# Performance work log

Hardware: AMD Instinct MI355X
Metric: run time of the kernel (lower is better)

## Reference

```python
import jax, jax.numpy as jnp
import numpy as np

B, S, EMBED, FFN, NQ = 8, 2048, 1024, 4096, 8

def setup_inputs() -> dict:
    key = jax.random.key(0)
    ks = jax.random.split(key, 6)
    return {
        "x": jax.random.normal(ks[0], (B, S, EMBED), dtype=jnp.float32),
        "theta": jax.random.normal(ks[1], (NQ,), dtype=jnp.float32),
        "W1": jax.random.normal(ks[2], (FFN, NQ), dtype=jnp.float32) * (1.0 / np.sqrt(NQ)),
        "b1": jax.random.normal(ks[3], (FFN,), dtype=jnp.float32) * 0.02,
        "W2": jax.random.normal(ks[4], (EMBED, FFN), dtype=jnp.float32) * (1.0 / np.sqrt(FFN)),
        "b2": jax.random.normal(ks[5], (EMBED,), dtype=jnp.float32) * 0.02,
    }

def reference(x, theta, W1, b1, W2, b2):
    # Quantum layer (product circuit, closed form): per qubit i,
    # |0> -RX(x_i)-> -RY(theta_i)->, <PauliZ> = cos(x_i) * cos(theta_i).
    nq = theta.shape[0]
    q = jnp.cos(x[..., :nq]) * jnp.cos(theta)        # [B,S,NQ]
    # dropout is identity in eval mode
    h = jax.nn.relu(jnp.einsum('bsq,fq->bsf', q, W1) + b1)  # [B,S,FFN]
    return jnp.einsum('bsf,ef->bse', h, W2) + b2            # [B,S,EMBED]
```

## Files before the change

### kernel.cpp

```cpp
#include <hip/hip_runtime.h>
#include <cstdint>
#include <cstddef>

#define AS1 __attribute__((address_space(1)))
#define AS3 __attribute__((address_space(3)))

typedef __bf16 bf16x8 __attribute__((ext_vector_type(8)));
typedef float  f32x16 __attribute__((ext_vector_type(16)));

#define MDIM 16384
#define NDIM 1024
#define KDIM 4096
#define NQ   8

#define BM 256
#define BN 256
#define BK 64

__global__ __launch_bounds__(256) void conv_w2_kernel(const float* __restrict__ W2,
                                                      __bf16* __restrict__ W2b) {
    size_t base = ((size_t)blockIdx.x * 256 + threadIdx.x) * 8;
    float4 a = *(const float4*)(W2 + base);
    float4 b = *(const float4*)(W2 + base + 4);
    bf16x8 v;
    v[0] = (__bf16)a.x; v[1] = (__bf16)a.y; v[2] = (__bf16)a.z; v[3] = (__bf16)a.w;
    v[4] = (__bf16)b.x; v[5] = (__bf16)b.y; v[6] = (__bf16)b.z; v[7] = (__bf16)b.w;
    *(bf16x8*)(W2b + base) = v;
}

#define QROWS 64
__global__ __launch_bounds__(256) void qh_kernel(const float* __restrict__ x,
                                                 const float* __restrict__ theta,
                                                 const float* __restrict__ W1,
                                                 const float* __restrict__ b1,
                                                 __bf16* __restrict__ H) {
    const int t  = threadIdx.x;
    const int f0 = blockIdx.y * 2048 + t * 8;
    const int r0 = blockIdx.x * QROWS;

    float w[8][8];
#pragma unroll
    for (int fr = 0; fr < 8; ++fr) {
        float4 a = *(const float4*)(W1 + (size_t)(f0 + fr) * NQ);
        float4 b = *(const float4*)(W1 + (size_t)(f0 + fr) * NQ + 4);
        w[fr][0] = a.x; w[fr][1] = a.y; w[fr][2] = a.z; w[fr][3] = a.w;
        w[fr][4] = b.x; w[fr][5] = b.y; w[fr][6] = b.z; w[fr][7] = b.w;
    }
    float bias[8];
    {
        float4 a = *(const float4*)(b1 + f0);
        float4 b = *(const float4*)(b1 + f0 + 4);
        bias[0] = a.x; bias[1] = a.y; bias[2] = a.z; bias[3] = a.w;
        bias[4] = b.x; bias[5] = b.y; bias[6] = b.z; bias[7] = b.w;
    }
    float ct[NQ];
#pragma unroll
    for (int i = 0; i < NQ; ++i) ct[i] = __cosf(theta[i]);

#pragma unroll 1
    for (int r = 0; r < QROWS; ++r) {
        const float* xr = x + (size_t)(r0 + r) * 1024;
        const float4 xa = *(const float4*)xr;
        const float4 xb = *(const float4*)(xr + 4);
        float q[8];
        q[0] = __cosf(xa.x) * ct[0]; q[1] = __cosf(xa.y) * ct[1];
        q[2] = __cosf(xa.z) * ct[2]; q[3] = __cosf(xa.w) * ct[3];
        q[4] = __cosf(xb.x) * ct[4]; q[5] = __cosf(xb.y) * ct[5];
        q[6] = __cosf(xb.z) * ct[6]; q[7] = __cosf(xb.w) * ct[7];
        bf16x8 o;
#pragma unroll
        for (int fr = 0; fr < 8; ++fr) {
            float a = bias[fr];
#pragma unroll
            for (int i = 0; i < 8; ++i) a += q[i] * w[fr][i];
            a = fmaxf(a, 0.f);
            o[fr] = (__bf16)a;
        }
        *(bf16x8*)(H + (size_t)(r0 + r) * KDIM + f0) = o;
    }
}

__global__ __launch_bounds__(256, 1) void gemm_bt_kernel(const __bf16* __restrict__ A,
                                                         const __bf16* __restrict__ B,
                                                         const float* __restrict__ bias,
                                                         float* __restrict__ C) {
    __shared__ __align__(16) __bf16 Al[BM * BK];
    __shared__ __align__(16) __bf16 Bl[BN * BK];

    const int tid  = threadIdx.x;
    const int wave = tid >> 6;
    const int lane = tid & 63;
    const int bm = blockIdx.x;
    const int bn = blockIdx.y;

    const int lr = lane >> 3;
    const int ul = (lane & 7) ^ lr;
    const __bf16* gA0 = A + (size_t)(bm * BM + wave * 64 + lr) * KDIM + ul * 8;
    const __bf16* gB0 = B + (size_t)(bn * BN + wave * 64 + lr) * KDIM + ul * 8;
    __bf16* lA0 = &Al[(wave * 64) * BK];
    __bf16* lB0 = &Bl[(wave * 64) * BK];

    const int fl = lane & 31;
    const int fq = lane >> 5;
    const int sw = fl & 7;
    const int wm = (wave & 1) * 128;
    const int wn = (wave >> 1) * 128;

    f32x16 acc[4][4] = {};

    for (int kt = 0; kt < KDIM; kt += BK) {
        __syncthreads();
#pragma unroll
        for (int c = 0; c < 8; ++c) {
            __builtin_amdgcn_global_load_lds((AS1 void*)(gA0 + (size_t)c * 8 * KDIM + kt),
                                             (AS3 void*)(lA0 + c * 8 * BK), 16, 0, 0);
            __builtin_amdgcn_global_load_lds((AS1 void*)(gB0 + (size_t)c * 8 * KDIM + kt),
                                             (AS3 void*)(lB0 + c * 8 * BK), 16, 0, 0);
        }
        __syncthreads();
#pragma unroll
        for (int t4 = 0; t4 < 4; ++t4) {
            const int u = ((t4 * 2 + fq) ^ sw) * 8;
            bf16x8 af[4], bfr[4];
#pragma unroll
            for (int i = 0; i < 4; ++i) {
                af[i]  = *(const bf16x8*)&Al[(wm + i * 32 + fl) * BK + u];
                bfr[i] = *(const bf16x8*)&Bl[(wn + i * 32 + fl) * BK + u];
            }
#pragma unroll
            for (int i = 0; i < 4; ++i)
#pragma unroll
                for (int j = 0; j < 4; ++j)
                    acc[i][j] = __builtin_amdgcn_mfma_f32_32x32x16_bf16(af[i], bfr[j], acc[i][j], 0, 0, 0);
        }
    }

    const int cm0 = bm * BM + wm;
    const int cn0 = bn * BN + wn;
#pragma unroll
    for (int j = 0; j < 4; ++j) {
        const int col = cn0 + j * 32 + fl;
        const float bv = bias[col];
#pragma unroll
        for (int i = 0; i < 4; ++i)
#pragma unroll
            for (int r = 0; r < 16; ++r) {
                const int row = cm0 + i * 32 + (r & 3) + 8 * (r >> 2) + 4 * fq;
                C[(size_t)row * NDIM + col] = acc[i][j][r] + bv;
            }
    }
}

extern "C" void kernel_launch(void* const* d_in, const int* in_sizes, int n_in,
                              void* d_out, int out_size, void* d_ws, size_t ws_size,
                              hipStream_t stream) {
    const float* x     = (const float*)d_in[0];
    const float* theta = (const float*)d_in[1];
    const float* W1    = (const float*)d_in[2];
    const float* b1    = (const float*)d_in[3];
    const float* W2    = (const float*)d_in[4];
    const float* b2    = (const float*)d_in[5];
    float* out = (float*)d_out;

    __bf16* H   = (__bf16*)d_ws;
    __bf16* W2b = (__bf16*)((char*)d_ws + (size_t)MDIM * KDIM * 2);

    conv_w2_kernel<<<(KDIM * NDIM) / (256 * 8), 256, 0, stream>>>(W2, W2b);
    qh_kernel<<<dim3(MDIM / QROWS, KDIM / 2048), 256, 0, stream>>>(x, theta, W1, b1, H);
    gemm_bt_kernel<<<dim3(MDIM / BM, NDIM / BN), 256, 0, stream>>>(H, W2b, b2, out);
}
```

Baseline: 332.1 us.

## Shrink GEMM tiles to 128x128 with 16x16 MFMA and restructure qh kernel

The GEMM block tile drops from 256x256 to 128x128, switches from 32x32x16 to 16x16x32 bf16 MFMA, raises launch bounds to allow three blocks per CU, and swaps the grid order so N-blocks vary fastest. This gives 1024 blocks instead of 256, aiming for better CU occupancy and L2 reuse of A rows on the 256-CU part. In exchange each block reuses less data from LDS and moves more traffic per flop. The qh kernel now computes q once per row into shared memory and loops over both FFN halves inside one block, removing the repeated cos computation.

Result: faster. 323.8 us (-2.5%).

```diff
diff --git a/kernel.cpp b/kernel.cpp
--- a/kernel.cpp
+++ b/kernel.cpp
@@ -6,15 +6,15 @@
 #define AS3 __attribute__((address_space(3)))
 
 typedef __bf16 bf16x8 __attribute__((ext_vector_type(8)));
-typedef float  f32x16 __attribute__((ext_vector_type(16)));
+typedef float  f32x4  __attribute__((ext_vector_type(4)));
 
 #define MDIM 16384
 #define NDIM 1024
 #define KDIM 4096
 #define NQ   8
 
-#define BM 256
-#define BN 256
+#define BM 128
+#define BN 128
 #define BK 64
 
 __global__ __launch_bounds__(256) void conv_w2_kernel(const float* __restrict__ W2,
@@ -28,59 +28,60 @@
     *(bf16x8*)(W2b + base) = v;
 }
 
-#define QROWS 64
+#define QROWS 32
 __global__ __launch_bounds__(256) void qh_kernel(const float* __restrict__ x,
                                                  const float* __restrict__ theta,
                                                  const float* __restrict__ W1,
                                                  const float* __restrict__ b1,
                                                  __bf16* __restrict__ H) {
+    __shared__ __align__(16) float qs[QROWS][NQ];
     const int t  = threadIdx.x;
-    const int f0 = blockIdx.y * 2048 + t * 8;
     const int r0 = blockIdx.x * QROWS;
 
-    float w[8][8];
+    {
+        const int qr = t >> 3, qi = t & 7;
+        const float xv = x[(size_t)(r0 + qr) * 1024 + qi];
+        qs[qr][qi] = __cosf(xv) * __cosf(theta[qi]);
+    }
+    __syncthreads();
+
 #pragma unroll
-    for (int fr = 0; fr < 8; ++fr) {
-        float4 a = *(const float4*)(W1 + (size_t)(f0 + fr) * NQ);
-        float4 b = *(const float4*)(W1 + (size_t)(f0 + fr) * NQ + 4);
-        w[fr][0] = a.x; w[fr][1] = a.y; w[fr][2] = a.z; w[fr][3] = a.w;
-        w[fr][4] = b.x; w[fr][5] = b.y; w[fr][6] = b.z; w[fr][7] = b.w;
-    }
-    float bias[8];
-    {
-        float4 a = *(const float4*)(b1 + f0);
-        float4 b = *(const float4*)(b1 + f0 + 4);
-        bias[0] = a.x; bias[1] = a.y; bias[2] = a.z; bias[3] = a.w;
-        bias[4] = b.x; bias[5] = b.y; bias[6] = b.z; bias[7] = b.w;
-    }
-    float ct[NQ];
-#pragma unroll
-    for (int i = 0; i < NQ; ++i) ct[i] = __cosf(theta[i]);
-
-#pragma unroll 1
-    for (int r = 0; r < QROWS; ++r) {
-        const float* xr = x + (size_t)(r0 + r) * 1024;
-        const float4 xa = *(const float4*)xr;
-        const float4 xb = *(const float4*)(xr + 4);
-        float q[8];
-        q[0] = __cosf(xa.x) * ct[0]; q[1] = __cosf(xa.y) * ct[1];
-        q[2] = __cosf(xa.z) * ct[2]; q[3] = __cosf(xa.w) * ct[3];
-        q[4] = __cosf(xb.x) * ct[4]; q[5] = __cosf(xb.y) * ct[5];
-        q[6] = __cosf(xb.z) * ct[6]; q[7] = __cosf(xb.w) * ct[7];
-        bf16x8 o;
+    for (int fc = 0; fc < 2; ++fc) {
+        const int f0 = fc * 2048 + t * 8;
+        float w[8][8];
 #pragma unroll
         for (int fr = 0; fr < 8; ++fr) {
-            float a = bias[fr];
+            float4 a = *(const float4*)(W1 + (size_t)(f0 + fr) * NQ);
+            float4 b = *(const float4*)(W1 + (size_t)(f0 + fr) * NQ + 4);
+            w[fr][0] = a.x; w[fr][1] = a.y; w[fr][2] = a.z; w[fr][3] = a.w;
+            w[fr][4] = b.x; w[fr][5] = b.y; w[fr][6] = b.z; w[fr][7] = b.w;
+        }
+        float bias[8];
+        {
+            float4 a = *(const float4*)(b1 + f0);
+            float4 b = *(const float4*)(b1 + f0 + 4);
+            bias[0] = a.x; bias[1] = a.y; bias[2] = a.z; bias[3] = a.w;
+            bias[4] = b.x; bias[5] = b.y; bias[6] = b.z; bias[7] = b.w;
+        }
+#pragma unroll 1
+        for (int r = 0; r < QROWS; ++r) {
+            const float4 qa = *(const float4*)&qs[r][0];
+            const float4 qb = *(const float4*)&qs[r][4];
+            float q[8] = { qa.x, qa.y, qa.z, qa.w, qb.x, qb.y, qb.z, qb.w };
+            bf16x8 o;
 #pragma unroll
-            for (int i = 0; i < 8; ++i) a += q[i] * w[fr][i];
-            a = fmaxf(a, 0.f);
-            o[fr] = (__bf16)a;
+            for (int fr = 0; fr < 8; ++fr) {
+                float a = bias[fr];
+#pragma unroll
+                for (int i = 0; i < 8; ++i) a += q[i] * w[fr][i];
+                o[fr] = (__bf16)fmaxf(a, 0.f);
+            }
+            *(bf16x8*)(H + (size_t)(r0 + r) * KDIM + f0) = o;
         }
-        *(bf16x8*)(H + (size_t)(r0 + r) * KDIM + f0) = o;
     }
 }
 
-__global__ __launch_bounds__(256, 1) void gemm_bt_kernel(const __bf16* __restrict__ A,
+__global__ __launch_bounds__(256, 3) void gemm_bt_kernel(const __bf16* __restrict__ A,
                                                          const __bf16* __restrict__ B,
                                                          const float* __restrict__ bias,
                                                          float* __restrict__ C) {
@@ -90,28 +91,28 @@
     const int tid  = threadIdx.x;
     const int wave = tid >> 6;
     const int lane = tid & 63;
-    const int bm = blockIdx.x;
-    const int bn = blockIdx.y;
+    const int bn = blockIdx.x;
+    const int bm = blockIdx.y;
 
     const int lr = lane >> 3;
     const int ul = (lane & 7) ^ lr;
-    const __bf16* gA0 = A + (size_t)(bm * BM + wave * 64 + lr) * KDIM + ul * 8;
-    const __bf16* gB0 = B + (size_t)(bn * BN + wave * 64 + lr) * KDIM + ul * 8;
-    __bf16* lA0 = &Al[(wave * 64) * BK];
-    __bf16* lB0 = &Bl[(wave * 64) * BK];
+    const __bf16* gA0 = A + (size_t)(bm * BM + wave * 32 + lr) * KDIM + ul * 8;
+    const __bf16* gB0 = B + (size_t)(bn * BN + wave * 32 + lr) * KDIM + ul * 8;
+    __bf16* lA0 = &Al[(wave * 32) * BK];
+    __bf16* lB0 = &Bl[(wave * 32) * BK];
 
-    const int fl = lane & 31;
-    const int fq = lane >> 5;
-    const int sw = fl & 7;
-    const int wm = (wave & 1) * 128;
-    const int wn = (wave >> 1) * 128;
+    const int ml = lane & 15;
+    const int kq = lane >> 4;
+    const int sw = lane & 7;
+    const int wm = (wave & 1) * 64;
+    const int wn = (wave >> 1) * 64;
 
-    f32x16 acc[4][4] = {};
+    f32x4 acc[4][4] = {};
 
     for (int kt = 0; kt < KDIM; kt += BK) {
         __syncthreads();
 #pragma unroll
-        for (int c = 0; c < 8; ++c) {
+        for (int c = 0; c < 4; ++c) {
             __builtin_amdgcn_global_load_lds((AS1 void*)(gA0 + (size_t)c * 8 * KDIM + kt),
                                              (AS3 void*)(lA0 + c * 8 * BK), 16, 0, 0);
             __builtin_amdgcn_global_load_lds((AS1 void*)(gB0 + (size_t)c * 8 * KDIM + kt),
@@ -119,19 +120,19 @@
         }
         __syncthreads();
 #pragma unroll
-        for (int t4 = 0; t4 < 4; ++t4) {
-            const int u = ((t4 * 2 + fq) ^ sw) * 8;
-            bf16x8 af[4], bfr[4];
+        for (int s = 0; s < 2; ++s) {
+            const int u = ((s * 4 + kq) ^ sw) * 8;
+            bf16x8 afrag[4], bfrag[4];
 #pragma unroll
             for (int i = 0; i < 4; ++i) {
-                af[i]  = *(const bf16x8*)&Al[(wm + i * 32 + fl) * BK + u];
-                bfr[i] = *(const bf16x8*)&Bl[(wn + i * 32 + fl) * BK + u];
+                afrag[i] = *(const bf16x8*)&Al[(wm + i * 16 + ml) * BK + u];
+                bfrag[i] = *(const bf16x8*)&Bl[(wn + i * 16 + ml) * BK + u];
             }
 #pragma unroll
             for (int i = 0; i < 4; ++i)
 #pragma unroll
                 for (int j = 0; j < 4; ++j)
-                    acc[i][j] = __builtin_amdgcn_mfma_f32_32x32x16_bf16(af[i], bfr[j], acc[i][j], 0, 0, 0);
+                    acc[i][j] = __builtin_amdgcn_mfma_f32_16x16x32_bf16(afrag[i], bfrag[j], acc[i][j], 0, 0, 0);
         }
     }
 
@@ -139,15 +140,15 @@
     const int cn0 = bn * BN + wn;
 #pragma unroll
     for (int j = 0; j < 4; ++j) {
-        const int col = cn0 + j * 32 + fl;
+        const int col = cn0 + j * 16 + ml;
         const float bv = bias[col];
 #pragma unroll
-        for (int i = 0; i < 4; ++i)
+        for (int i = 0; i < 4; ++i) {
+            const int row0 = cm0 + i * 16 + kq * 4;
 #pragma unroll
-            for (int r = 0; r < 16; ++r) {
-                const int row = cm0 + i * 32 + (r & 3) + 8 * (r >> 2) + 4 * fq;
-                C[(size_t)row * NDIM + col] = acc[i][j][r] + bv;
-            }
+            for (int r = 0; r < 4; ++r)
+                C[(size_t)(row0 + r) * NDIM + col] = acc[i][j][r] + bv;
+        }
     }
 }
 
@@ -166,6 +167,6 @@
     __bf16* W2b = (__bf16*)((char*)d_ws + (size_t)MDIM * KDIM * 2);
 
     conv_w2_kernel<<<(KDIM * NDIM) / (256 * 8), 256, 0, stream>>>(W2, W2b);
-    qh_kernel<<<dim3(MDIM / QROWS, KDIM / 2048), 256, 0, stream>>>(x, theta, W1, b1, H);
-    gemm_bt_kernel<<<dim3(MDIM / BM, NDIM / BN), 256, 0, stream>>>(H, W2b, b2, out);
+    qh_kernel<<<MDIM / QROWS, 256, 0, stream>>>(x, theta, W1, b1, H);
+    gemm_bt_kernel<<<dim3(NDIM / BN, MDIM / BM), 256, 0, stream>>>(H, W2b, b2, out);
 }
```
